# Performance work log

Measured on AMD Instinct MI355X. Metric: run time of the kernel, lower is better.

Reference implementation:

```python
import jax, jax.numpy as jnp
import numpy as np

N_NODES = 100000
N_EDGES = 3200000
C_IN = 128
C_OUT = 64
HEADS = 1
NEG_SLOPE = 0.2  # GraphLayer attention leaky_relu
OUT_SLOPE = 0.01  # nn.LeakyReLU default in GATLayer
BN_EPS = 1e-5


def setup_inputs() -> dict:
    key = jax.random.key(0)
    ks = jax.random.split(key, 12)
    x = jax.random.normal(ks[0], (N_NODES, C_IN), dtype=jnp.float32)
    src = jax.random.randint(ks[1], (N_EDGES,), 0, N_NODES, dtype=jnp.int32)
    # guarantee no self loops so remove_self_loops is a no-op (static shapes)
    off = jax.random.randint(ks[2], (N_EDGES,), 0, N_NODES - 1, dtype=jnp.int32)
    dst = (src + 1 + off) % N_NODES
    edge_index = jnp.stack([src, dst])  # [2, E], row0=src(j), row1=dst(i)
    embedding = jax.random.normal(ks[3], (N_NODES, C_OUT), dtype=jnp.float32)
    lin_w = jax.random.normal(ks[4], (HEADS * C_OUT, C_IN), dtype=jnp.float32) / np.sqrt(C_IN)
    lin_b = jax.random.normal(ks[5], (HEADS * C_OUT,), dtype=jnp.float32) * 0.02
    att_i = jax.random.normal(ks[6], (1, HEADS, C_OUT), dtype=jnp.float32) / np.sqrt(C_OUT)
    att_j = jax.random.normal(ks[7], (1, HEADS, C_OUT), dtype=jnp.float32) / np.sqrt(C_OUT)
    att_em_i = jax.random.normal(ks[8], (1, HEADS, C_OUT), dtype=jnp.float32) / np.sqrt(C_OUT)
    att_em_j = jax.random.normal(ks[9], (1, HEADS, C_OUT), dtype=jnp.float32) / np.sqrt(C_OUT)
    bias = jax.random.normal(ks[10], (C_OUT,), dtype=jnp.float32) * 0.02
    bn_gamma = jax.random.uniform(ks[11], (C_OUT,), dtype=jnp.float32, minval=0.5, maxval=1.5)
    bn_beta = jax.random.normal(jax.random.fold_in(key, 99), (C_OUT,), dtype=jnp.float32) * 0.1
    return {"x": x, "edge_index": edge_index, "embedding": embedding,
            "lin_w": lin_w, "lin_b": lin_b,
            "att_i": att_i, "att_j": att_j,
            "att_em_i": att_em_i, "att_em_j": att_em_j,
            "bias": bias, "bn_gamma": bn_gamma, "bn_beta": bn_beta}


def reference(x, edge_index, embedding, lin_w, lin_b,
              att_i, att_j, att_em_i, att_em_j, bias, bn_gamma, bn_beta):
    N = x.shape[0]
    H, Co = att_i.shape[1], att_i.shape[2]
    node_num = N  # GATLayer passes node_num == number of nodes

    xl = (x @ lin_w.T + lin_b).reshape(N, H, Co)  # lin(x) -> [N,H,Co]

    # add self loops (input edges contain none)
    ar = jnp.arange(N, dtype=edge_index.dtype)
    src = jnp.concatenate([edge_index[0], ar])  # j
    dst = jnp.concatenate([edge_index[1], ar])  # i (target / edge_index_i)

    # per-node attention scores; alpha_e = s_i[dst] + s_j[src]
    # (key_i . cat_att_i) = x_i.att_i + emb_i.att_em_i  -- depends only on node
    emb_h = embedding[:, None, :]  # [N,1,Co] broadcast over heads
    s_i = (xl * att_i).sum(-1) + (emb_h * att_em_i).sum(-1)  # [N,H]
    s_j = (xl * att_j).sum(-1) + (emb_h * att_em_j).sum(-1)  # [N,H]

    emb_idx_i = dst % node_num  # identity here, kept for faithfulness
    emb_idx_j = src % node_num
    alpha = (xl[dst] * att_i).sum(-1) * 0  # placeholder removed below
    alpha = s_i[emb_idx_i] * 0 + s_i[dst] + s_j[src]  # [E,H]
    alpha = jax.nn.leaky_relu(alpha, NEG_SLOPE)

    # segment softmax over target node (dst)
    amax = jax.ops.segment_max(alpha, dst, num_segments=N)  # [N,H]
    ex = jnp.exp(alpha - amax[dst])
    denom = jax.ops.segment_sum(ex, dst, num_segments=N)
    alpha = ex / denom[dst]  # [E,H]

    # weighted messages + scatter-sum aggregate (dropout p=0)
    msg = xl[src] * alpha[:, :, None]  # [E,H,Co]
    agg = jax.ops.segment_sum(msg, dst, num_segments=N)  # [N,H,Co]

    out = agg.mean(axis=1) + bias  # concat=False -> mean over heads, [N,Co]

    # BatchNorm1d (training-mode batch stats, biased variance)
    mu = out.mean(axis=0)
    var = ((out - mu) ** 2).mean(axis=0)
    out = bn_gamma * (out - mu) * jax.lax.rsqrt(var + BN_EPS) + bn_beta
    out = jax.nn.leaky_relu(out, OUT_SLOPE)

    att_weight = alpha[:, :, None]  # [E,H,1], matches returned alpha
    return out, att_weight
```

## Files before the change

### kernel.cpp

```cpp
#include <hip/hip_runtime.h>
#include <hip/hip_bf16.h>

#define CIN 128
#define CO  64

typedef __attribute__((ext_vector_type(8))) short shortx8;
typedef __attribute__((ext_vector_type(4))) float floatx4;

__device__ __forceinline__ float lrelu(float x, float s) { return x > 0.f ? x : x * s; }

__device__ __forceinline__ short f2bs(float f) {
    union { __hip_bfloat16 h; short s; } u;
    u.h = __float2bfloat16(f);
    return u.s;
}

__device__ __forceinline__ shortx8 pack8(const float4& a, const float4& b) {
    shortx8 r;
    r[0] = f2bs(a.x); r[1] = f2bs(a.y); r[2] = f2bs(a.z); r[3] = f2bs(a.w);
    r[4] = f2bs(b.x); r[5] = f2bs(b.y); r[6] = f2bs(b.z); r[7] = f2bs(b.w);
    return r;
}

__global__ __launch_bounds__(256) void k_escore(
    const float* __restrict__ emb, const float* __restrict__ aei, const float* __restrict__ aej,
    float* __restrict__ sie, float* __restrict__ sje, int N)
{
    int lane = threadIdx.x & 63;
    int slot = lane & 15, grp = lane >> 4;
    float4 vi = ((const float4*)aei)[slot];
    float4 vj = ((const float4*)aej)[slot];
    int w = blockIdx.x * 4 + (threadIdx.x >> 6);
    int nwaves = gridDim.x * 4;
    int groups = (N + 3) >> 2;
    for (int g = w; g < groups; g += nwaves) {
        int n = g * 4 + grp;
        float pi = 0.f, pj = 0.f;
        if (n < N) {
            float4 e = ((const float4*)(emb + (size_t)n * CO))[slot];
            pi = e.x * vi.x + e.y * vi.y + e.z * vi.z + e.w * vi.w;
            pj = e.x * vj.x + e.y * vj.y + e.z * vj.z + e.w * vj.w;
        }
#pragma unroll
        for (int off = 1; off < 16; off <<= 1) {
            pi += __shfl_xor(pi, off);
            pj += __shfl_xor(pj, off);
        }
        if (slot == 0 && n < N) { sie[n] = pi; sje[n] = pj; }
    }
}

__global__ __launch_bounds__(256) void k_gemm(
    const float* __restrict__ x, const float* __restrict__ W,
    const float* __restrict__ lb, const float* __restrict__ ai, const float* __restrict__ aj,
    const float* __restrict__ sie, const float* __restrict__ sje,
    __hip_bfloat16* __restrict__ xlb, float* __restrict__ s_i, float* __restrict__ s_j, int N)
{
    __shared__ __hip_bfloat16 tile[4][16 * 72];
    const int lane = threadIdx.x & 63;
    const int wv   = threadIdx.x >> 6;
    const int col0 = lane & 15;
    const int quad = lane >> 4;

    shortx8 wf[4][4];
#pragma unroll
    for (int cg = 0; cg < 4; ++cg)
#pragma unroll
        for (int ks = 0; ks < 4; ++ks) {
            const float* wp = W + (cg * 16 + col0) * CIN + ks * 32 + quad * 8;
            float4 w0 = *(const float4*)wp;
            float4 w1 = *(const float4*)(wp + 4);
            wf[cg][ks] = pack8(w0, w1);
        }
    float biasv[4], aiv[4], ajv[4];
#pragma unroll
    for (int cg = 0; cg < 4; ++cg) {
        biasv[cg] = lb[cg * 16 + col0];
        aiv[cg]   = ai[cg * 16 + col0];
        ajv[cg]   = aj[cg * 16 + col0];
    }

    int tiles = (N + 15) >> 4;
    for (int t = blockIdx.x * 4 + wv; t < tiles; t += gridDim.x * 4) {
        int n0 = t * 16;
        int arow = n0 + col0; if (arow > N - 1) arow = N - 1;
        const float* xp = x + (size_t)arow * CIN + quad * 8;
        float4 a0[4], a1[4];
#pragma unroll
        for (int ks = 0; ks < 4; ++ks) {
            a0[ks] = *(const float4*)(xp + ks * 32);
            a1[ks] = *(const float4*)(xp + ks * 32 + 4);
        }
        floatx4 z = {0.f, 0.f, 0.f, 0.f};
        floatx4 acc[4] = {z, z, z, z};
#pragma unroll
        for (int ks = 0; ks < 4; ++ks) {
            shortx8 af = pack8(a0[ks], a1[ks]);
#pragma unroll
            for (int cg = 0; cg < 4; ++cg)
                acc[cg] = __builtin_amdgcn_mfma_f32_16x16x32_bf16(af, wf[cg][ks], acc[cg], 0, 0, 0);
        }
        float pi[4] = {0, 0, 0, 0}, pj[4] = {0, 0, 0, 0};
        __hip_bfloat16* tp = tile[wv];
#pragma unroll
        for (int cg = 0; cg < 4; ++cg)
#pragma unroll
            for (int r = 0; r < 4; ++r) {
                float v = acc[cg][r] + biasv[cg];
                pi[r] = fmaf(v, aiv[cg], pi[r]);
                pj[r] = fmaf(v, ajv[cg], pj[r]);
                tp[(quad * 4 + r) * 72 + cg * 16 + col0] = __float2bfloat16(v);
            }
        __asm__ __volatile__("s_waitcnt lgkmcnt(0)" ::: "memory");
        int rr = lane >> 2, hh = lane & 3;
        int orow = n0 + rr;
        if (orow < N) {
            const float4* sp = (const float4*)(tp + rr * 72 + hh * 16);
            float4 v0 = sp[0], v1 = sp[1];
            float4* gp = (float4*)(xlb + (size_t)orow * CO + hh * 16);
            gp[0] = v0; gp[1] = v1;
        }
#pragma unroll
        for (int r = 0; r < 4; ++r)
#pragma unroll
            for (int off = 1; off < 16; off <<= 1) {
                pi[r] += __shfl_xor(pi[r], off);
                pj[r] += __shfl_xor(pj[r], off);
            }
        if (col0 == 0) {
#pragma unroll
            for (int r = 0; r < 4; ++r) {
                int n = n0 + quad * 4 + r;
                if (n < N) {
                    s_i[n] = sie[n] + pi[r];
                    s_j[n] = sje[n] + pj[r];
                }
            }
        }
    }
}

#define BIN_CHUNK 8192
__global__ __launch_bounds__(512) void k_binA(
    const int* __restrict__ src, const int* __restrict__ dst, int E, int CAP,
    int* __restrict__ gcur, unsigned* __restrict__ ebuf)
{
    __shared__ int hist[1024];
    __shared__ int lscan[1024];
    __shared__ int gofs[1024];
    __shared__ int wsum[8];
    __shared__ int wbase[8];
    __shared__ unsigned sbuf[BIN_CHUNK];
    __shared__ unsigned short sbid[BIN_CHUNK];
    int base = blockIdx.x * BIN_CHUNK;
    int cnt  = min(BIN_CHUNK, E - base);
    int t = threadIdx.x;
    int lane = t & 63, wid = t >> 6;

    hist[2 * t]     = 0;
    hist[2 * t + 1] = 0;
    __syncthreads();
    for (int k = t; k < cnt; k += 512) atomicAdd(&hist[dst[base + k] >> 7], 1);
    __syncthreads();

    int h0 = hist[2 * t], h1 = hist[2 * t + 1];
    int v = h0 + h1;
#pragma unroll
    for (int off = 1; off < 64; off <<= 1) {
        int y = __shfl_up(v, off);
        if (lane >= off) v += y;
    }
    if (lane == 63) wsum[wid] = v;
    __syncthreads();
    if (t == 0) {
        int a = 0;
#pragma unroll
        for (int i = 0; i < 8; ++i) { wbase[i] = a; a += wsum[i]; }
    }
    __syncthreads();
    int excl = v + wbase[wid] - (h0 + h1);
    lscan[2 * t]     = excl;
    lscan[2 * t + 1] = excl + h0;
    __syncthreads();

    for (int b = t; b < 1024; b += 512) {
        int c = hist[b];
        if (c) gofs[b] = b * CAP + atomicAdd(&gcur[b], c) - lscan[b];
        hist[b] = 0;
    }
    __syncthreads();

    for (int k = t; k < cnt; k += 512) {
        int d = dst[base + k];
        int s = src[base + k];
        int b = d >> 7;
        unsigned packed = (unsigned)s | ((unsigned)(d & 127) << 17);
        int loc = lscan[b] + atomicAdd(&hist[b], 1);
        sbuf[loc] = packed;
        sbid[loc] = (unsigned short)b;
    }
    __syncthreads();

    for (int k = t; k < cnt; k += 512) {
        int b = sbid[k];
        ebuf[gofs[b] + k] = sbuf[k];
    }
}

#define CAPMAX 6272
__global__ __launch_bounds__(256) void k_binB(
    const unsigned* __restrict__ ebuf, const int* __restrict__ gcur,
    const float* __restrict__ s_i, const float* __restrict__ s_j,
    int2* __restrict__ rowse, uint2* __restrict__ epair, int N, int CAP)
{
    __shared__ int h[128];
    __shared__ int sc[128];
    __shared__ int lloc[128];
    __shared__ int lcur[128];
    __shared__ float sil[128];
    __shared__ uint2 sbuf[CAPMAX];
    int b = blockIdx.x;
    int start = b << 7;
    int sz = min(128, N - start);
    int eb   = b * CAP;
    int ep0  = b * (CAP + 128);
    int cntB = gcur[b];
    int t = threadIdx.x;
    if (t < 128) { h[t] = 0; lcur[t] = 0; }
    if (t < sz) sil[t] = s_i[start + t];
    __syncthreads();
    for (int k = t; k < cntB; k += 256) atomicAdd(&h[ebuf[eb + k] >> 17], 1);
    __syncthreads();
    if (t < 128) sc[t] = h[t];
    __syncthreads();
    for (int off = 1; off < 128; off <<= 1) {
        int y = (t >= off && t < 128) ? sc[t - off] : 0;
        __syncthreads();
        if (t < 128) sc[t] += y;
        __syncthreads();
    }
    if (t < sz) {
        int l = (sc[t] - h[t]) + t;
        lloc[t] = l;
        rowse[start + t] = make_int2(ep0 + l, h[t] + 1);
        float a  = sil[t] + s_j[start + t];
        float ev = __expf(a > 0.f ? a : 0.2f * a);
        sbuf[l + h[t]] = make_uint2((unsigned)(start + t), __float_as_uint(ev));
    }
    __syncthreads();
    for (int k = t; k < cntB; k += 256) {
        unsigned e = ebuf[eb + k];
        int doff = (int)(e >> 17);
        int s    = (int)(e & 0x1FFFFu);
        float a  = sil[doff] + s_j[s];
        float ev = __expf(a > 0.f ? a : 0.2f * a);
        int p = atomicAdd(&lcur[doff], 1);
        sbuf[lloc[doff] + p] = make_uint2((unsigned)s, __float_as_uint(ev));
    }
    __syncthreads();
    int tot = cntB + sz;
    for (int k = t; k < tot; k += 256)
        epair[ep0 + k] = sbuf[k];
}

__global__ __launch_bounds__(256) void k_agg(
    const __hip_bfloat16* __restrict__ xlb,
    const float* __restrict__ s_i,
    const int2* __restrict__ rowse, const uint2* __restrict__ epair,
    const float* __restrict__ bias, int N,
    float* __restrict__ outp, float2* __restrict__ pd,
    float* __restrict__ spread)
{
    __shared__ float r1s[4][64];
    __shared__ float r2s[4][64];
    int lane = threadIdx.x & 63;
    int wv   = threadIdx.x >> 6;
    int n    = blockIdx.x * 4 + wv;
    int grp  = lane >> 3;
    int q    = lane & 7;

    float acc[8] = {0, 0, 0, 0, 0, 0, 0, 0};
    float den = 0.f;
    float val[8] = {0, 0, 0, 0, 0, 0, 0, 0};

    if (n < N) {
        int2 se = rowse[n];
        int r0 = se.x, cnt = se.y;
        float si_n = s_i[n];
        const uint2* pp = epair + r0;
        const unsigned short* xb = (const unsigned short*)xlb;

        auto PROC = [&](uint2 p) {
            float w = __uint_as_float(p.y);
            uint4 g = *(const uint4*)(xb + ((size_t)p.x << 6) + (q << 3));
            den += w;
            acc[0] = fmaf(w, __uint_as_float(g.x << 16),          acc[0]);
            acc[1] = fmaf(w, __uint_as_float(g.x & 0xffff0000u),  acc[1]);
            acc[2] = fmaf(w, __uint_as_float(g.y << 16),          acc[2]);
            acc[3] = fmaf(w, __uint_as_float(g.y & 0xffff0000u),  acc[3]);
            acc[4] = fmaf(w, __uint_as_float(g.z << 16),          acc[4]);
            acc[5] = fmaf(w, __uint_as_float(g.z & 0xffff0000u),  acc[5]);
            acc[6] = fmaf(w, __uint_as_float(g.w << 16),          acc[6]);
            acc[7] = fmaf(w, __uint_as_float(g.w & 0xffff0000u),  acc[7]);
        };

        int cnt16 = cnt & ~15;
        if (cnt16 > 0) {
            uint2 c0 = pp[grp];
            uint2 c1 = pp[8 + grp];
            int k = 0;
            for (; k + 16 < cnt16; k += 16) {
                uint2 n0 = pp[k + 16 + grp];
                uint2 n1 = pp[k + 24 + grp];
                PROC(c0);
                PROC(c1);
                c0 = n0; c1 = n1;
            }
            PROC(c0);
            PROC(c1);
        }
        for (int idx = cnt16 + grp; idx < cnt; idx += 8) {
            uint2 p = pp[idx];
            PROC(p);
        }

#pragma unroll
        for (int j = 0; j < 8; ++j) {
            acc[j] += __shfl_xor(acc[j], 8);
            acc[j] += __shfl_xor(acc[j], 16);
            acc[j] += __shfl_xor(acc[j], 32);
        }
        den += __shfl_xor(den, 8);
        den += __shfl_xor(den, 16);
        den += __shfl_xor(den, 32);

        float inv = 1.0f / den;
#pragma unroll
        for (int j = 0; j < 8; ++j)
            val[j] = acc[j] * inv + bias[q * 8 + j];

        if (grp == 0) {
            float4 v0 = make_float4(val[0], val[1], val[2], val[3]);
            float4 v1 = make_float4(val[4], val[5], val[6], val[7]);
            float* op = outp + (size_t)n * CO + q * 8;
            ((float4*)op)[0] = v0;
            ((float4*)op)[1] = v1;
        }
        if (lane == 0) pd[n] = make_float2(si_n, inv);
    }
    if (grp == 0) {
#pragma unroll
        for (int j = 0; j < 8; ++j) {
            r1s[wv][q * 8 + j] = val[j];
            r2s[wv][q * 8 + j] = val[j] * val[j];
        }
    }
    __syncthreads();
    if (threadIdx.x < 64) {
        int l = threadIdx.x;
        float s1 = r1s[0][l] + r1s[1][l] + r1s[2][l] + r1s[3][l];
        float s2 = r2s[0][l] + r2s[1][l] + r2s[2][l] + r2s[3][l];
        int slot = blockIdx.x & 255;
        atomicAdd(&spread[slot * 128 + l],      s1);
        atomicAdd(&spread[slot * 128 + 64 + l], s2);
    }
}

__global__ void k_att(const int* __restrict__ src, const int* __restrict__ dst, int E, int N,
                      const float2* __restrict__ pd, const float* __restrict__ s_j,
                      float* __restrict__ att)
{
    int i = blockIdx.x * 256 + threadIdx.x;
    int tot = E + N;
    if (i >= tot) return;
    int s, d;
    if (i < E) { s = src[i]; d = dst[i]; } else { s = d = i - E; }
    float2 p = pd[d];
    float a = lrelu(p.x + s_j[s], 0.2f);
    att[i] = __expf(a) * p.y;
}

__global__ __launch_bounds__(1024) void k_bnstats(const float* __restrict__ spread, int N,
    const float* __restrict__ gamma, const float* __restrict__ beta,
    float* __restrict__ scale, float* __restrict__ shift)
{
    __shared__ float red[8][128];
    __shared__ float tot[128];
    int c = threadIdx.x & 127;
    int p = threadIdx.x >> 7;
    float a = 0.f;
    for (int s = p; s < 256; s += 8) a += spread[s * 128 + c];
    red[p][c] = a;
    __syncthreads();
    if (threadIdx.x < 128) {
        float t = 0.f;
        for (int q = 0; q < 8; ++q) t += red[q][c];
        tot[c] = t;
    }
    __syncthreads();
    if (threadIdx.x < 64) {
        float inv = 1.f / (float)N;
        float mu  = tot[threadIdx.x] * inv;
        float msq = tot[64 + threadIdx.x] * inv;
        float var = msq - mu * mu;
        float sc  = gamma[threadIdx.x] * rsqrtf(var + 1e-5f);
        scale[threadIdx.x] = sc;
        shift[threadIdx.x] = beta[threadIdx.x] - mu * sc;
    }
}

__global__ void k_bnapply(float* __restrict__ outp, int N,
                          const float* __restrict__ scale, const float* __restrict__ shift)
{
    int i = blockIdx.x * 256 + threadIdx.x;
    int tot = N * CO / 4;
    if (i >= tot) return;
    float4 v = ((float4*)outp)[i];
    int c0 = (i * 4) & (CO - 1);
    v.x = lrelu(fmaf(scale[c0 + 0], v.x, shift[c0 + 0]), 0.01f);
    v.y = lrelu(fmaf(scale[c0 + 1], v.y, shift[c0 + 1]), 0.01f);
    v.z = lrelu(fmaf(scale[c0 + 2], v.z, shift[c0 + 2]), 0.01f);
    v.w = lrelu(fmaf(scale[c0 + 3], v.w, shift[c0 + 3]), 0.01f);
    ((float4*)outp)[i] = v;
}

extern "C" void kernel_launch(void* const* d_in, const int* in_sizes, int n_in,
                              void* d_out, int out_size, void* d_ws, size_t ws_size,
                              hipStream_t stream)
{
    const float* x    = (const float*)d_in[0];
    const int*   ei   = (const int*)  d_in[1];
    const float* emb  = (const float*)d_in[2];
    const float* W    = (const float*)d_in[3];
    const float* lb   = (const float*)d_in[4];
    const float* ai   = (const float*)d_in[5];
    const float* aj   = (const float*)d_in[6];
    const float* aei  = (const float*)d_in[7];
    const float* aej  = (const float*)d_in[8];
    const float* bias = (const float*)d_in[9];
    const float* gam  = (const float*)d_in[10];
    const float* bet  = (const float*)d_in[11];

    int N = in_sizes[0] / CIN;
    int E = in_sizes[1] / 2;
    const int* srcv = ei;
    const int* dstv = ei + E;
    int NBUK = (N + 127) >> 7;

    int avg = (E + NBUK - 1) / NBUK;
    int CAP = ((avg * 3 / 2) + 255) & ~255;
    if (CAP + 128 > CAPMAX) CAP = CAPMAX - 128;

    float* ws = (float*)d_ws;
    size_t o = 0;
    __hip_bfloat16* xlb = (__hip_bfloat16*)(ws + o); o += (size_t)N * CO / 2;
    float* s_i   = ws + o; o += N;
    float* s_j   = ws + o; o += N;
    float* sie   = ws + o; o += N;
    float* sje   = ws + o; o += N;
    float2* pd   = (float2*)(ws + o); o += 2 * (size_t)N;
    int2*  rowse = (int2*)(ws + o); o += 2 * (size_t)N;
    size_t zoff  = o;
    int*   gcur  = (int*)(ws + o); o += 1024;
    float* spread= ws + o;         o += 256 * 128;
    size_t zbytes = (o - zoff) * sizeof(float);
    float* scale = ws + o; o += CO;
    float* shift = ws + o; o += CO;
    unsigned* ebuf = (unsigned*)(ws + o); o += (size_t)NBUK * CAP;
    uint2* epair = (uint2*)(ws + o); o += 2 * ((size_t)NBUK * (CAP + 128)) + 64;

    float* out_nodes = (float*)d_out;
    float* out_att   = out_nodes + (size_t)N * CO;

    hipMemsetAsync((void*)gcur, 0, zbytes, stream);

    int CHB = (E + BIN_CHUNK - 1) / BIN_CHUNK;
    k_escore<<<1024, 256, 0, stream>>>(emb, aei, aej, sie, sje, N);
    k_gemm<<<512, 256, 0, stream>>>(x, W, lb, ai, aj, sie, sje, xlb, s_i, s_j, N);
    k_binA<<<CHB, 512, 0, stream>>>(srcv, dstv, E, CAP, gcur, ebuf);
    k_binB<<<NBUK, 256, 0, stream>>>(ebuf, gcur, s_i, s_j, rowse, epair, N, CAP);
    k_agg<<<(N + 3) / 4, 256, 0, stream>>>(xlb, s_i, rowse, epair, bias, N,
                                           out_nodes, pd, spread);
    k_att<<<(E + N + 255) / 256, 256, 0, stream>>>(srcv, dstv, E, N, pd, s_j, out_att);
    k_bnstats<<<1, 1024, 0, stream>>>(spread, N, gam, bet, scale, shift);
    k_bnapply<<<((N * CO / 4) + 255) / 256, 256, 0, stream>>>(out_nodes, N, scale, shift);
}
```

Baseline: 341.8 us.

## Fuse embedding scores into GEMM and move edge exp from binning to aggregation

The separate embedding-score kernel is removed and its dot products are computed inside the GEMM kernel, saving a launch and a round trip through the sie/sje buffers. The binning kernel now stores only sorted source indices (4 bytes per edge instead of 8), and the aggregation kernel gathers s_j[src] and recomputes the leaky-relu exp per edge. This halves the sorted edge-array traffic but adds a random 4-byte gather per edge in the aggregation inner loop. The aggregation prefetch pipeline depth also drops from 16 to 8 edges.

```diff
diff --git a/kernel.cpp b/kernel.cpp
--- a/kernel.cpp
+++ b/kernel.cpp
@@ -22,38 +22,10 @@
     return r;
 }
 
-__global__ __launch_bounds__(256) void k_escore(
-    const float* __restrict__ emb, const float* __restrict__ aei, const float* __restrict__ aej,
-    float* __restrict__ sie, float* __restrict__ sje, int N)
-{
-    int lane = threadIdx.x & 63;
-    int slot = lane & 15, grp = lane >> 4;
-    float4 vi = ((const float4*)aei)[slot];
-    float4 vj = ((const float4*)aej)[slot];
-    int w = blockIdx.x * 4 + (threadIdx.x >> 6);
-    int nwaves = gridDim.x * 4;
-    int groups = (N + 3) >> 2;
-    for (int g = w; g < groups; g += nwaves) {
-        int n = g * 4 + grp;
-        float pi = 0.f, pj = 0.f;
-        if (n < N) {
-            float4 e = ((const float4*)(emb + (size_t)n * CO))[slot];
-            pi = e.x * vi.x + e.y * vi.y + e.z * vi.z + e.w * vi.w;
-            pj = e.x * vj.x + e.y * vj.y + e.z * vj.z + e.w * vj.w;
-        }
-#pragma unroll
-        for (int off = 1; off < 16; off <<= 1) {
-            pi += __shfl_xor(pi, off);
-            pj += __shfl_xor(pj, off);
-        }
-        if (slot == 0 && n < N) { sie[n] = pi; sje[n] = pj; }
-    }
-}
-
 __global__ __launch_bounds__(256) void k_gemm(
     const float* __restrict__ x, const float* __restrict__ W,
     const float* __restrict__ lb, const float* __restrict__ ai, const float* __restrict__ aj,
-    const float* __restrict__ sie, const float* __restrict__ sje,
+    const float* __restrict__ emb, const float* __restrict__ aei, const float* __restrict__ aej,
     __hip_bfloat16* __restrict__ xlb, float* __restrict__ s_i, float* __restrict__ s_j, int N)
 {
     __shared__ __hip_bfloat16 tile[4][16 * 72];
@@ -79,6 +51,8 @@
         aiv[cg]   = ai[cg * 16 + col0];
         ajv[cg]   = aj[cg * 16 + col0];
     }
+    float4 ei4 = ((const float4*)aei)[col0];
+    float4 ej4 = ((const float4*)aej)[col0];
 
     int tiles = (N + 15) >> 4;
     for (int t = blockIdx.x * 4 + wv; t < tiles; t += gridDim.x * 4) {
@@ -111,6 +85,13 @@
                 pj[r] = fmaf(v, ajv[cg], pj[r]);
                 tp[(quad * 4 + r) * 72 + cg * 16 + col0] = __float2bfloat16(v);
             }
+#pragma unroll
+        for (int r = 0; r < 4; ++r) {
+            int nr = n0 + quad * 4 + r; if (nr > N - 1) nr = N - 1;
+            float4 e = ((const float4*)(emb + (size_t)nr * CO))[col0];
+            pi[r] += e.x * ei4.x + e.y * ei4.y + e.z * ei4.z + e.w * ei4.w;
+            pj[r] += e.x * ej4.x + e.y * ej4.y + e.z * ej4.z + e.w * ej4.w;
+        }
         __asm__ __volatile__("s_waitcnt lgkmcnt(0)" ::: "memory");
         int rr = lane >> 2, hh = lane & 3;
         int orow = n0 + rr;
@@ -132,8 +113,8 @@
             for (int r = 0; r < 4; ++r) {
                 int n = n0 + quad * 4 + r;
                 if (n < N) {
-                    s_i[n] = sie[n] + pi[r];
-                    s_j[n] = sje[n] + pj[r];
+                    s_i[n] = pi[r];
+                    s_j[n] = pj[r];
                 }
             }
         }
@@ -210,15 +191,13 @@
 #define CAPMAX 6272
 __global__ __launch_bounds__(256) void k_binB(
     const unsigned* __restrict__ ebuf, const int* __restrict__ gcur,
-    const float* __restrict__ s_i, const float* __restrict__ s_j,
-    int2* __restrict__ rowse, uint2* __restrict__ epair, int N, int CAP)
+    int2* __restrict__ rowse, int* __restrict__ ssort, int N, int CAP)
 {
     __shared__ int h[128];
     __shared__ int sc[128];
     __shared__ int lloc[128];
     __shared__ int lcur[128];
-    __shared__ float sil[128];
-    __shared__ uint2 sbuf[CAPMAX];
+    __shared__ int sbuf[CAPMAX];
     int b = blockIdx.x;
     int start = b << 7;
     int sz = min(128, N - start);
@@ -227,7 +206,6 @@
     int cntB = gcur[b];
     int t = threadIdx.x;
     if (t < 128) { h[t] = 0; lcur[t] = 0; }
-    if (t < sz) sil[t] = s_i[start + t];
     __syncthreads();
     for (int k = t; k < cntB; k += 256) atomicAdd(&h[ebuf[eb + k] >> 17], 1);
     __syncthreads();
@@ -243,30 +221,26 @@
         int l = (sc[t] - h[t]) + t;
         lloc[t] = l;
         rowse[start + t] = make_int2(ep0 + l, h[t] + 1);
-        float a  = sil[t] + s_j[start + t];
-        float ev = __expf(a > 0.f ? a : 0.2f * a);
-        sbuf[l + h[t]] = make_uint2((unsigned)(start + t), __float_as_uint(ev));
+        sbuf[l + h[t]] = start + t;
     }
     __syncthreads();
     for (int k = t; k < cntB; k += 256) {
         unsigned e = ebuf[eb + k];
         int doff = (int)(e >> 17);
         int s    = (int)(e & 0x1FFFFu);
-        float a  = sil[doff] + s_j[s];
-        float ev = __expf(a > 0.f ? a : 0.2f * a);
         int p = atomicAdd(&lcur[doff], 1);
-        sbuf[lloc[doff] + p] = make_uint2((unsigned)s, __float_as_uint(ev));
+        sbuf[lloc[doff] + p] = s;
     }
     __syncthreads();
     int tot = cntB + sz;
     for (int k = t; k < tot; k += 256)
-        epair[ep0 + k] = sbuf[k];
+        ssort[ep0 + k] = sbuf[k];
 }
 
 __global__ __launch_bounds__(256) void k_agg(
     const __hip_bfloat16* __restrict__ xlb,
-    const float* __restrict__ s_i,
-    const int2* __restrict__ rowse, const uint2* __restrict__ epair,
+    const float* __restrict__ s_i, const float* __restrict__ s_j,
+    const int2* __restrict__ rowse, const int* __restrict__ ssort,
     const float* __restrict__ bias, int N,
     float* __restrict__ outp, float2* __restrict__ pd,
     float* __restrict__ spread)
@@ -287,12 +261,13 @@
         int2 se = rowse[n];
         int r0 = se.x, cnt = se.y;
         float si_n = s_i[n];
-        const uint2* pp = epair + r0;
+        const int* sp = ssort + r0;
         const unsigned short* xb = (const unsigned short*)xlb;
 
-        auto PROC = [&](uint2 p) {
-            float w = __uint_as_float(p.y);
-            uint4 g = *(const uint4*)(xb + ((size_t)p.x << 6) + (q << 3));
+        auto GATHER = [&](int s) -> uint4 {
+            return *(const uint4*)(xb + ((size_t)s << 6) + (q << 3));
+        };
+        auto PROC = [&](float w, uint4 g) {
             den += w;
             acc[0] = fmaf(w, __uint_as_float(g.x << 16),          acc[0]);
             acc[1] = fmaf(w, __uint_as_float(g.x & 0xffff0000u),  acc[1]);
@@ -304,24 +279,29 @@
             acc[7] = fmaf(w, __uint_as_float(g.w & 0xffff0000u),  acc[7]);
         };
 
-        int cnt16 = cnt & ~15;
-        if (cnt16 > 0) {
-            uint2 c0 = pp[grp];
-            uint2 c1 = pp[8 + grp];
+        int cnt8 = cnt & ~7;
+        if (cnt8 > 0) {
+            int   s_c  = sp[grp];
+            uint4 g_c  = GATHER(s_c);
+            float sj_c = s_j[s_c];
             int k = 0;
-            for (; k + 16 < cnt16; k += 16) {
-                uint2 n0 = pp[k + 16 + grp];
-                uint2 n1 = pp[k + 24 + grp];
-                PROC(c0);
-                PROC(c1);
-                c0 = n0; c1 = n1;
+            for (; k + 16 <= cnt8; k += 8) {
+                int   s_n  = sp[k + 8 + grp];
+                uint4 g_n  = GATHER(s_n);
+                float sj_n = s_j[s_n];
+                float a = si_n + sj_c;
+                PROC(__expf(a > 0.f ? a : 0.2f * a), g_c);
+                g_c = g_n; sj_c = sj_n;
             }
-            PROC(c0);
-            PROC(c1);
-        }
-        for (int idx = cnt16 + grp; idx < cnt; idx += 8) {
-            uint2 p = pp[idx];
-            PROC(p);
+            float a = si_n + sj_c;
+            PROC(__expf(a > 0.f ? a : 0.2f * a), g_c);
+        }
+        for (int idx = cnt8 + grp; idx < cnt; idx += 8) {
+            int s = sp[idx];
+            float sj = s_j[s];
+            uint4 g = GATHER(s);
+            float a = si_n + sj;
+            PROC(__expf(a > 0.f ? a : 0.2f * a), g);
         }
 
 #pragma unroll
@@ -456,8 +436,6 @@
     __hip_bfloat16* xlb = (__hip_bfloat16*)(ws + o); o += (size_t)N * CO / 2;
     float* s_i   = ws + o; o += N;
     float* s_j   = ws + o; o += N;
-    float* sie   = ws + o; o += N;
-    float* sje   = ws + o; o += N;
     float2* pd   = (float2*)(ws + o); o += 2 * (size_t)N;
     int2*  rowse = (int2*)(ws + o); o += 2 * (size_t)N;
     size_t zoff  = o;
@@ -467,7 +445,7 @@
     float* scale = ws + o; o += CO;
     float* shift = ws + o; o += CO;
     unsigned* ebuf = (unsigned*)(ws + o); o += (size_t)NBUK * CAP;
-    uint2* epair = (uint2*)(ws + o); o += 2 * ((size_t)NBUK * (CAP + 128)) + 64;
+    int*   ssort = (int*)(ws + o); o += (size_t)NBUK * (CAP + 128) + 64;
 
     float* out_nodes = (float*)d_out;
     float* out_att   = out_nodes + (size_t)N * CO;
@@ -475,11 +453,10 @@
     hipMemsetAsync((void*)gcur, 0, zbytes, stream);
 
     int CHB = (E + BIN_CHUNK - 1) / BIN_CHUNK;
-    k_escore<<<1024, 256, 0, stream>>>(emb, aei, aej, sie, sje, N);
-    k_gemm<<<512, 256, 0, stream>>>(x, W, lb, ai, aj, sie, sje, xlb, s_i, s_j, N);
+    k_gemm<<<512, 256, 0, stream>>>(x, W, lb, ai, aj, emb, aei, aej, xlb, s_i, s_j, N);
     k_binA<<<CHB, 512, 0, stream>>>(srcv, dstv, E, CAP, gcur, ebuf);
-    k_binB<<<NBUK, 256, 0, stream>>>(ebuf, gcur, s_i, s_j, rowse, epair, N, CAP);
-    k_agg<<<(N + 3) / 4, 256, 0, stream>>>(xlb, s_i, rowse, epair, bias, N,
+    k_binB<<<NBUK, 256, 0, stream>>>(ebuf, gcur, rowse, ssort, N, CAP);
+    k_agg<<<(N + 3) / 4, 256, 0, stream>>>(xlb, s_i, s_j, rowse, ssort, bias, N,
                                            out_nodes, pd, spread);
     k_att<<<(E + N + 255) / 256, 256, 0, stream>>>(srcv, dstv, E, N, pd, s_j, out_att);
     k_bnstats<<<1, 1024, 0, stream>>>(spread, N, gam, bet, scale, shift);
```

Measured after the change: 312.7 us. -8.5%, faster.
